# Kernel tuning notes

Hardware: AMD Instinct MI355X
Metric: run time of the kernel (lower is better)

The kernel has to match this reference:

```python
import jax, jax.numpy as jnp
import numpy as np

B, S, D = 32, 512, 1024  # batch, seq_len, input_dim == output_dim


def setup_inputs() -> dict:
    key = jax.random.key(0)
    ks = jax.random.split(key, 13)
    std = 0.05  # tf.random_normal_initializer default stddev
    w = lambda k, shp: (jax.random.normal(k, shp, dtype=jnp.float32) * std)
    inp = {"seq_input_vec": jax.random.normal(ks[0], (B, S, D), dtype=jnp.float32)}
    names = ["Ui", "Wi", "Uf", "Wf", "Uo", "Wo", "Ug", "Wg"]
    for i, n in enumerate(names):
        inp[n] = w(ks[1 + i], (D, D))
    for n in ["bi", "bf", "bo", "bg"]:
        inp[n] = jnp.zeros((D,), dtype=jnp.float32)
    return inp


def reference(seq_input_vec, Ui, Wi, bi, Uf, Wf, bf, Uo, Wo, bo, Ug, Wg, bg):
    # seq_input_vec: [B, S, D]. Fuse the 4 input projections into one GEMM
    # over the whole sequence (mathematically identical to per-step matmuls).
    U = jnp.concatenate([Ui, Uf, Uo, Ug], axis=1)          # [D, 4D]
    W = jnp.concatenate([Wi, Wf, Wo, Wg], axis=1)          # [D, 4D]
    b = jnp.concatenate([bi, bf, bo, bg], axis=0)          # [4D]
    x_proj = jnp.einsum('bsd,de->sbe', seq_input_vec, U) + b  # [S, B, 4D]

    d = seq_input_vec.shape[-1]
    h0 = jnp.zeros((seq_input_vec.shape[0], d), dtype=seq_input_vec.dtype)
    c0 = jnp.zeros_like(h0)

    def step(carry, xp):
        c_prev, h_prev = carry
        z = xp + h_prev @ W                                 # [B, 4D]
        zi, zf, zo, zg = jnp.split(z, 4, axis=-1)
        i_t = jax.nn.sigmoid(zi)
        f_t = jax.nn.sigmoid(zf)
        o_t = jax.nn.sigmoid(zo)
        g_t = jnp.tanh(zg)
        # NOTE: original (nonstandard) math applies sigmoid to the cell update
        c_t = jax.nn.sigmoid(f_t * c_prev + i_t * g_t)
        h_t = jnp.tanh(c_t) * o_t
        return (c_t, h_t), h_t

    _, hs = jax.lax.scan(step, (c0, h0), x_proj)            # hs: [S, B, D]
    return jnp.transpose(hs, (1, 0, 2))                     # [B, S, D]
```

## Files before the change

### kernel.cpp

```cpp
#include <hip/hip_runtime.h>

typedef unsigned int u32;
typedef unsigned short u16;
typedef unsigned long long u64;
typedef __attribute__((ext_vector_type(8))) short short8;
typedef __attribute__((ext_vector_type(4))) float f32x4;

#define SEQ 512
#define BATCH 32
#define DIM 1024
#define NB 128

#define OFF_XT    0ull
#define OFF_UBT   33554432ull
#define OFF_WG2   41943040ull
#define OFF_XPROJ 50331648ull
#define OFF_HBUF  184549376ull
#define OFF_BIAS  184680448ull
#define OFF_SYNC  184696832ull

__device__ __forceinline__ float bf2f(u16 u) {
  union { u32 u; float f; } v; v.u = ((u32)u) << 16; return v.f;
}
__device__ __forceinline__ u16 f2bf(float f) {
  union { float f; u32 u; } v; v.f = f;
  u32 r = v.u + 0x7FFFu + ((v.u >> 16) & 1u);
  return (u16)(r >> 16);
}
__device__ __forceinline__ float tanh_fast(float x) {
  return 1.f - 2.f / (1.f + __expf(2.f * x));
}
__device__ __forceinline__ void gload_lds16(const u16* g, u16* l) {
  __builtin_amdgcn_global_load_lds(
      (const __attribute__((address_space(1))) u32*)g,
      (__attribute__((address_space(3))) u32*)l, 16, 0, 0);
}
__device__ __forceinline__ void gload_lds16_coh(const u16* g, u16* l) {
  __builtin_amdgcn_global_load_lds(
      (const __attribute__((address_space(1))) u32*)g,
      (__attribute__((address_space(3))) u32*)l, 16, 0, 17);
}

__global__ void k_init(u32* hb, float* biasc, u32* sync,
                       const float* bi, const float* bfv,
                       const float* bo, const float* bg) {
  int i = blockIdx.x * 256 + threadIdx.x;
  if (i < 32768) {
    hb[i] = 0u;
  } else if (i < 32768 + 4096) {
    int e = i - 32768;
    int g = e >> 10, c = e & 1023;
    const float* p = (g == 0) ? bi : (g == 1) ? bfv : (g == 2) ? bo : bg;
    biasc[e] = p[c];
  } else if (i < 32768 + 4096 + 4096) {
    sync[i - 32768 - 4096] = 0u;
  }
}

__global__ void k_prep_w(const float* Ui, const float* Wi, const float* Uf,
                         const float* Wf, const float* Uo, const float* Wo,
                         const float* Ug, const float* Wg, u16* Ubt, u16* Wg2) {
  __shared__ float tile[64][65];
  int bx = blockIdx.x;
  int mi = bx >> 8;
  int tt = bx & 255;
  int tr = tt >> 4, tc = tt & 15;
  const float* src;
  switch (mi) {
    case 0: src = Ui; break; case 1: src = Wi; break;
    case 2: src = Uf; break; case 3: src = Wf; break;
    case 4: src = Uo; break; case 5: src = Wo; break;
    case 6: src = Ug; break; default: src = Wg; break;
  }
  int g = mi >> 1;
  int d0 = tr * 64, c0 = tc * 64;
  int ty = threadIdx.x >> 6, tx = threadIdx.x & 63;
#pragma unroll
  for (int i = 0; i < 16; ++i) {
    int r = i * 4 + ty;
    tile[r][tx] = src[(size_t)(d0 + r) * 1024 + c0 + tx];
  }
  __syncthreads();
  if (mi & 1) {
#pragma unroll
    for (int i = 0; i < 16; ++i) {
      int cc = i * 4 + ty;
      int c_full = c0 + cc;
      int k = d0 + tx;
      int blk = c_full >> 3;
      int rr = (g << 3) | (c_full & 7);
      Wg2[(size_t)blk * 32768 + ((k >> 5) << 10) + rr * 32 + (k & 31)] =
          f2bf(tile[tx][cc]);
    }
  } else {
#pragma unroll
    for (int i = 0; i < 16; ++i) {
      int cc = i * 4 + ty;
      Ubt[(size_t)((g << 10) + c0 + cc) * 1024 + d0 + tx] = f2bf(tile[tx][cc]);
    }
  }
}

__global__ void k_prep_x(const float* __restrict__ X, u16* __restrict__ Xt) {
  int idx = blockIdx.x * 256 + threadIdx.x;
  int m = idx >> 8, d4 = (idx & 255) << 2;
  int s = m >> 5, b = m & 31;
  const float4* p = (const float4*)(X + (size_t)(b * SEQ + s) * DIM + d4);
  float4 v = *p;
  u16 o[4] = { f2bf(v.x), f2bf(v.y), f2bf(v.z), f2bf(v.w) };
  *(ushort4*)(Xt + (size_t)m * DIM + d4) = *(ushort4*)o;
}

__global__ __launch_bounds__(256) void k_gemm(const u16* __restrict__ Xt,
                                              const u16* __restrict__ Ubt,
                                              const float* __restrict__ biasc,
                                              u16* __restrict__ xproj) {
  __shared__ u16 As[128 * 32];
  __shared__ u16 Bs[128 * 32];
  int tid = threadIdx.x;
  int w = tid >> 6, l = tid & 63;
  int n0 = blockIdx.x * 128, m0 = blockIdx.y * 128;
  int wm = w >> 1, wn = w & 1;
  int lrow = l & 15, lq = l >> 4;
  f32x4 acc[4][4] = {};
  for (int kt = 0; kt < 32; ++kt) {
    int k0 = kt * 32;
    __syncthreads();
#pragma unroll
    for (int is = 0; is < 2; ++is) {
      int c = is * 256 + w * 64 + l;
      int row = c >> 2, kg = c & 3;
      gload_lds16(Xt + (size_t)(m0 + row) * 1024 + k0 + kg * 8, As + c * 8);
      gload_lds16(Ubt + (size_t)(n0 + row) * 1024 + k0 + kg * 8, Bs + c * 8);
    }
    __syncthreads();
    short8 af[4], bf[4];
#pragma unroll
    for (int mt = 0; mt < 4; ++mt)
      af[mt] = *(const short8*)(As + (wm * 64 + mt * 16 + lrow) * 32 + lq * 8);
#pragma unroll
    for (int nt = 0; nt < 4; ++nt)
      bf[nt] = *(const short8*)(Bs + (wn * 64 + nt * 16 + lrow) * 32 + lq * 8);
#pragma unroll
    for (int mt = 0; mt < 4; ++mt)
#pragma unroll
      for (int nt = 0; nt < 4; ++nt)
        acc[mt][nt] = __builtin_amdgcn_mfma_f32_16x16x32_bf16(
            af[mt], bf[nt], acc[mt][nt], 0, 0, 0);
  }
#pragma unroll
  for (int nt = 0; nt < 4; ++nt) {
    int col = n0 + wn * 64 + nt * 16 + lrow;
    float bv = biasc[col];
#pragma unroll
    for (int mt = 0; mt < 4; ++mt) {
      int rbase = m0 + wm * 64 + mt * 16 + lq * 4;
#pragma unroll
      for (int r = 0; r < 4; ++r)
        xproj[(size_t)(rbase + r) * 4096 + col] = f2bf(acc[mt][nt][r] + bv);
    }
  }
}

__global__ __launch_bounds__(256, 1) void k_rec(const u16* __restrict__ Wg2,
                                                const u16* __restrict__ xproj,
                                                u16* hbuf, float* out, u32* sync) {
  __shared__ u16 Ws[32 * 1024];
  __shared__ u16 Hs[32 * 1024];
  __shared__ u16 XPs[32 * 32];
  __shared__ float zbuf[32][33];
  int tid = threadIdx.x;
  int w = tid >> 6, l = tid & 63;
  int blk = blockIdx.x;
  int lrow = l & 15, lq = l >> 4;
#pragma unroll
  for (int it = 0; it < 16; ++it) {
    int c = it * 256 + w * 64 + l;
    gload_lds16(Wg2 + (size_t)blk * 32768 + c * 8, Ws + c * 8);
  }
  if (w < 2) {
    int c2 = w * 64 + l;
    int b = c2 >> 2, g = c2 & 3;
    gload_lds16(xproj + (size_t)b * 4096 + (g << 10) + (blk << 3), XPs + c2 * 8);
  }
  float c_reg = 0.f;
  int eb = tid >> 3, ec = tid & 7;
  int mt = w >> 1, nt = w & 1;
  const u16* ap0 = Hs + (mt * 16 + lrow) * 32 + lq * 8;
  const u16* bp0 = Ws + (nt * 16 + lrow) * 32 + lq * 8;
  u16* hst_base = hbuf + ((blk >> 2) << 10) + eb * 32 + ((blk & 3) << 3) + ec;
  float* out_base = out + (size_t)eb * SEQ * DIM + (blk << 3) + ec;
  __syncthreads();

  for (int s = 0; s < SEQ; ++s) {
    {
      u32 tgt = (u32)s;
      int guard = 0;
      for (;;) {
        u32 a = __hip_atomic_load(sync + l * 32, __ATOMIC_RELAXED,
                                  __HIP_MEMORY_SCOPE_AGENT);
        u32 b = __hip_atomic_load(sync + (64 + l) * 32, __ATOMIC_RELAXED,
                                  __HIP_MEMORY_SCOPE_AGENT);
        if (a >= tgt && b >= tgt) break;
        __builtin_amdgcn_s_sleep(1);
        if (++guard > 20000000) break;
      }
    }
    asm volatile("" ::: "memory");

    const u16* hsrc = hbuf + (size_t)(s & 1) * 32768;
#pragma unroll
    for (int it = 0; it < 16; ++it) {
      int c = it * 256 + w * 64 + l;
      gload_lds16_coh(hsrc + c * 8, Hs + c * 8);
    }
    asm volatile("s_waitcnt vmcnt(8)" ::: "memory");
    __builtin_amdgcn_s_barrier();
    __builtin_amdgcn_sched_barrier(0);

    f32x4 acc0 = { 0.f, 0.f, 0.f, 0.f };
    f32x4 acc1 = { 0.f, 0.f, 0.f, 0.f };
#pragma unroll
    for (int ks = 0; ks < 8; ++ks) {
      short8 a0 = *(const short8*)(ap0 + (2 * ks) * 1024);
      short8 b0 = *(const short8*)(bp0 + (2 * ks) * 1024);
      short8 a1 = *(const short8*)(ap0 + (2 * ks + 1) * 1024);
      short8 b1 = *(const short8*)(bp0 + (2 * ks + 1) * 1024);
      acc0 = __builtin_amdgcn_mfma_f32_16x16x32_bf16(a0, b0, acc0, 0, 0, 0);
      acc1 = __builtin_amdgcn_mfma_f32_16x16x32_bf16(a1, b1, acc1, 0, 0, 0);
    }
    asm volatile("s_waitcnt vmcnt(0)" ::: "memory");
    __builtin_amdgcn_s_barrier();
    __builtin_amdgcn_sched_barrier(0);
#pragma unroll
    for (int ks = 8; ks < 16; ++ks) {
      short8 a0 = *(const short8*)(ap0 + (2 * ks) * 1024);
      short8 b0 = *(const short8*)(bp0 + (2 * ks) * 1024);
      short8 a1 = *(const short8*)(ap0 + (2 * ks + 1) * 1024);
      short8 b1 = *(const short8*)(bp0 + (2 * ks + 1) * 1024);
      acc0 = __builtin_amdgcn_mfma_f32_16x16x32_bf16(a0, b0, acc0, 0, 0, 0);
      acc1 = __builtin_amdgcn_mfma_f32_16x16x32_bf16(a1, b1, acc1, 0, 0, 0);
    }
    f32x4 acc = acc0 + acc1;
    {
      int col = nt * 16 + lrow;
      int rb = mt * 16 + lq * 4;
#pragma unroll
      for (int r = 0; r < 4; ++r) zbuf[rb + r][col] = acc[r];
    }
    __syncthreads();

    float zi = zbuf[eb][ec]      + bf2f(XPs[eb * 32 + ec]);
    float zf = zbuf[eb][8 + ec]  + bf2f(XPs[eb * 32 + 8 + ec]);
    float zo = zbuf[eb][16 + ec] + bf2f(XPs[eb * 32 + 16 + ec]);
    float zg = zbuf[eb][24 + ec] + bf2f(XPs[eb * 32 + 24 + ec]);
    float ig = 1.f / (1.f + __expf(-zi));
    float fg = 1.f / (1.f + __expf(-zf));
    float og = 1.f / (1.f + __expf(-zo));
    float gg = tanh_fast(zg);
    c_reg = 1.f / (1.f + __expf(-(fg * c_reg + ig * gg)));
    float h = tanh_fast(c_reg) * og;
    __hip_atomic_store(hst_base + (size_t)(((s + 1) & 1)) * 32768, f2bf(h),
                       __ATOMIC_RELAXED, __HIP_MEMORY_SCOPE_AGENT);
    __syncthreads();

    if (tid == 0)
      __hip_atomic_store(sync + blk * 32, (u32)(s + 1), __ATOMIC_RELAXED,
                         __HIP_MEMORY_SCOPE_AGENT);
    {
      int sp = (s + 1 < SEQ) ? s + 1 : s;
      if (w < 2) {
        int c2 = w * 64 + l;
        int b = c2 >> 2, g = c2 & 3;
        gload_lds16(xproj + (size_t)(sp * 32 + b) * 4096 + (g << 10) + (blk << 3),
                    XPs + c2 * 8);
      }
    }
    __builtin_nontemporal_store(h, out_base + (size_t)s * DIM);
  }
}

extern "C" void kernel_launch(void* const* d_in, const int* in_sizes, int n_in,
                              void* d_out, int out_size, void* d_ws,
                              size_t ws_size, hipStream_t stream) {
  const float* X   = (const float*)d_in[0];
  const float* Ui  = (const float*)d_in[1];
  const float* Wi  = (const float*)d_in[2];
  const float* Uf  = (const float*)d_in[3];
  const float* Wf  = (const float*)d_in[4];
  const float* Uo  = (const float*)d_in[5];
  const float* Wo  = (const float*)d_in[6];
  const float* Ug  = (const float*)d_in[7];
  const float* Wg  = (const float*)d_in[8];
  const float* bi  = (const float*)d_in[9];
  const float* bfv = (const float*)d_in[10];
  const float* bo  = (const float*)d_in[11];
  const float* bg  = (const float*)d_in[12];
  char* ws = (char*)d_ws;
  u16* Xt      = (u16*)(ws + OFF_XT);
  u16* Ubt     = (u16*)(ws + OFF_UBT);
  u16* Wg2     = (u16*)(ws + OFF_WG2);
  u16* xproj   = (u16*)(ws + OFF_XPROJ);
  u16* hbuf    = (u16*)(ws + OFF_HBUF);
  float* biasc = (float*)(ws + OFF_BIAS);
  u32* sync    = (u32*)(ws + OFF_SYNC);
  float* out   = (float*)d_out;

  k_init<<<160, 256, 0, stream>>>((u32*)hbuf, biasc, sync, bi, bfv, bo, bg);
  k_prep_w<<<2048, 256, 0, stream>>>(Ui, Wi, Uf, Wf, Uo, Wo, Ug, Wg, Ubt, Wg2);
  k_prep_x<<<16384, 256, 0, stream>>>(X, Xt);
  k_gemm<<<dim3(32, 128), 256, 0, stream>>>(Xt, Ubt, biasc, xproj);
  k_rec<<<NB, 256, 0, stream>>>(Wg2, xproj, hbuf, out, sync);
}
```

Before: 1.948 ms.

## Split recurrent block into two independent batch halves with per-half sync

The recurrent kernel now splits each block's 256 threads into two 128-thread groups, each handling 16 of the 32 batch rows. Each group waits on its own set of global step flags, loads only its half of h, and synchronises its two waves through an LDS flag spin instead of block-wide barriers. This lets the two batch halves advance through the sequence independently, so the cross-block dependency chain covers only half the batch. The cost is more flag traffic, spin-waiting on LDS flags, and double-buffered xproj staging. The bf array is also renamed to avoid shadowing a variable name.

Measured after the change: 2.688 ms. 38.0% more time.

```diff
diff --git a/kernel.cpp b/kernel.cpp
--- a/kernel.cpp
+++ b/kernel.cpp
@@ -39,6 +39,19 @@
   __builtin_amdgcn_global_load_lds(
       (const __attribute__((address_space(1))) u32*)g,
       (__attribute__((address_space(3))) u32*)l, 16, 0, 17);
+}
+
+__device__ __forceinline__ void half_sync(volatile u32* hsf, int g, int wv,
+                                          u32 ep) {
+  asm volatile("s_waitcnt lgkmcnt(0)" ::: "memory");
+  if ((threadIdx.x & 63) == 0) hsf[g * 2 + wv] = ep;
+  asm volatile("s_waitcnt lgkmcnt(0)" ::: "memory");
+  int guard = 0;
+  while (hsf[g * 2 + (wv ^ 1)] < ep) {
+    if (++guard > 100000000) break;
+  }
+  asm volatile("" ::: "memory");
+  __builtin_amdgcn_sched_barrier(0);
 }
 
 __global__ void k_init(u32* hb, float* biasc, u32* sync,
@@ -134,19 +147,19 @@
       gload_lds16(Ubt + (size_t)(n0 + row) * 1024 + k0 + kg * 8, Bs + c * 8);
     }
     __syncthreads();
-    short8 af[4], bf[4];
+    short8 af[4], bfr[4];
 #pragma unroll
     for (int mt = 0; mt < 4; ++mt)
       af[mt] = *(const short8*)(As + (wm * 64 + mt * 16 + lrow) * 32 + lq * 8);
 #pragma unroll
     for (int nt = 0; nt < 4; ++nt)
-      bf[nt] = *(const short8*)(Bs + (wn * 64 + nt * 16 + lrow) * 32 + lq * 8);
+      bfr[nt] = *(const short8*)(Bs + (wn * 64 + nt * 16 + lrow) * 32 + lq * 8);
 #pragma unroll
     for (int mt = 0; mt < 4; ++mt)
 #pragma unroll
       for (int nt = 0; nt < 4; ++nt)
         acc[mt][nt] = __builtin_amdgcn_mfma_f32_16x16x32_bf16(
-            af[mt], bf[nt], acc[mt][nt], 0, 0, 0);
+            af[mt], bfr[nt], acc[mt][nt], 0, 0, 0);
   }
 #pragma unroll
   for (int nt = 0; nt < 4; ++nt) {
@@ -166,30 +179,36 @@
                                                 const u16* __restrict__ xproj,
                                                 u16* hbuf, float* out, u32* sync) {
   __shared__ u16 Ws[32 * 1024];
-  __shared__ u16 Hs[32 * 1024];
-  __shared__ u16 XPs[32 * 32];
-  __shared__ float zbuf[32][33];
+  __shared__ u16 Hs[2][16 * 1024];
+  __shared__ u16 XPs[2][2][512];
+  __shared__ float zb[2][16][33];
+  __shared__ u32 hsf[4];
   int tid = threadIdx.x;
   int w = tid >> 6, l = tid & 63;
+  int g = tid >> 7;
+  int wv = w & 1;
   int blk = blockIdx.x;
   int lrow = l & 15, lq = l >> 4;
+  if (tid < 4) hsf[tid] = 0u;
 #pragma unroll
   for (int it = 0; it < 16; ++it) {
     int c = it * 256 + w * 64 + l;
     gload_lds16(Wg2 + (size_t)blk * 32768 + c * 8, Ws + c * 8);
   }
-  if (w < 2) {
-    int c2 = w * 64 + l;
-    int b = c2 >> 2, g = c2 & 3;
-    gload_lds16(xproj + (size_t)b * 4096 + (g << 10) + (blk << 3), XPs + c2 * 8);
+  {
+    int bloc = l >> 2, gs = l & 3;
+    gload_lds16(xproj + (size_t)(g * 16 + bloc) * 4096 + gs * 1024 + (blk << 3),
+                &XPs[g][0][l * 8]);
   }
   float c_reg = 0.f;
-  int eb = tid >> 3, ec = tid & 7;
-  int mt = w >> 1, nt = w & 1;
-  const u16* ap0 = Hs + (mt * 16 + lrow) * 32 + lq * 8;
-  const u16* bp0 = Ws + (nt * 16 + lrow) * 32 + lq * 8;
-  u16* hst_base = hbuf + ((blk >> 2) << 10) + eb * 32 + ((blk & 3) << 3) + ec;
-  float* out_base = out + (size_t)eb * SEQ * DIM + (blk << 3) + ec;
+  int eb = (tid & 127) >> 3, ec = tid & 7;
+  const u16* ap0 = Hs[g] + lrow * 32 + lq * 8;
+  const u16* bp0 = Ws + (wv * 16 + lrow) * 32 + lq * 8;
+  int d = (blk << 3) + ec;
+  u16* hst_base = hbuf + ((d >> 5) << 10) + (g * 16 + eb) * 32 + (d & 31);
+  float* out_base = out + (size_t)(g * 16 + eb) * SEQ * DIM + d;
+  const u32* syncg = sync + g * 2048;
+  u32 epc = 0;
   __syncthreads();
 
   for (int s = 0; s < SEQ; ++s) {
@@ -197,9 +216,9 @@
       u32 tgt = (u32)s;
       int guard = 0;
       for (;;) {
-        u32 a = __hip_atomic_load(sync + l * 32, __ATOMIC_RELAXED,
+        u32 a = __hip_atomic_load(syncg + l * 16, __ATOMIC_RELAXED,
                                   __HIP_MEMORY_SCOPE_AGENT);
-        u32 b = __hip_atomic_load(sync + (64 + l) * 32, __ATOMIC_RELAXED,
+        u32 b = __hip_atomic_load(syncg + (64 + l) * 16, __ATOMIC_RELAXED,
                                   __HIP_MEMORY_SCOPE_AGENT);
         if (a >= tgt && b >= tgt) break;
         __builtin_amdgcn_s_sleep(1);
@@ -208,75 +227,66 @@
     }
     asm volatile("" ::: "memory");
 
-    const u16* hsrc = hbuf + (size_t)(s & 1) * 32768;
-#pragma unroll
-    for (int it = 0; it < 16; ++it) {
-      int c = it * 256 + w * 64 + l;
-      gload_lds16_coh(hsrc + c * 8, Hs + c * 8);
-    }
-    asm volatile("s_waitcnt vmcnt(8)" ::: "memory");
-    __builtin_amdgcn_s_barrier();
+    const u16* hsrc = hbuf + (size_t)(s & 1) * 32768 + g * 512 + l * 8;
+#pragma unroll
+    for (int t = 0; t < 16; ++t) {
+      int tile = wv * 16 + t;
+      gload_lds16_coh(hsrc + tile * 1024, Hs[g] + tile * 512 + l * 8);
+    }
+    asm volatile("s_waitcnt vmcnt(0)" ::: "memory");
     __builtin_amdgcn_sched_barrier(0);
+    half_sync(hsf, g, wv, ++epc);
 
     f32x4 acc0 = { 0.f, 0.f, 0.f, 0.f };
     f32x4 acc1 = { 0.f, 0.f, 0.f, 0.f };
 #pragma unroll
-    for (int ks = 0; ks < 8; ++ks) {
-      short8 a0 = *(const short8*)(ap0 + (2 * ks) * 1024);
-      short8 b0 = *(const short8*)(bp0 + (2 * ks) * 1024);
-      short8 a1 = *(const short8*)(ap0 + (2 * ks + 1) * 1024);
-      short8 b1 = *(const short8*)(bp0 + (2 * ks + 1) * 1024);
+    for (int kk = 0; kk < 16; ++kk) {
+      short8 a0 = *(const short8*)(ap0 + (2 * kk) * 512);
+      short8 b0 = *(const short8*)(bp0 + (2 * kk) * 1024);
+      short8 a1 = *(const short8*)(ap0 + (2 * kk + 1) * 512);
+      short8 b1 = *(const short8*)(bp0 + (2 * kk + 1) * 1024);
       acc0 = __builtin_amdgcn_mfma_f32_16x16x32_bf16(a0, b0, acc0, 0, 0, 0);
       acc1 = __builtin_amdgcn_mfma_f32_16x16x32_bf16(a1, b1, acc1, 0, 0, 0);
     }
-    asm volatile("s_waitcnt vmcnt(0)" ::: "memory");
-    __builtin_amdgcn_s_barrier();
-    __builtin_amdgcn_sched_barrier(0);
-#pragma unroll
-    for (int ks = 8; ks < 16; ++ks) {
-      short8 a0 = *(const short8*)(ap0 + (2 * ks) * 1024);
-      short8 b0 = *(const short8*)(bp0 + (2 * ks) * 1024);
-      short8 a1 = *(const short8*)(ap0 + (2 * ks + 1) * 1024);
-      short8 b1 = *(const short8*)(bp0 + (2 * ks + 1) * 1024);
-      acc0 = __builtin_amdgcn_mfma_f32_16x16x32_bf16(a0, b0, acc0, 0, 0, 0);
-      acc1 = __builtin_amdgcn_mfma_f32_16x16x32_bf16(a1, b1, acc1, 0, 0, 0);
-    }
     f32x4 acc = acc0 + acc1;
     {
-      int col = nt * 16 + lrow;
-      int rb = mt * 16 + lq * 4;
-#pragma unroll
-      for (int r = 0; r < 4; ++r) zbuf[rb + r][col] = acc[r];
-    }
-    __syncthreads();
-
-    float zi = zbuf[eb][ec]      + bf2f(XPs[eb * 32 + ec]);
-    float zf = zbuf[eb][8 + ec]  + bf2f(XPs[eb * 32 + 8 + ec]);
-    float zo = zbuf[eb][16 + ec] + bf2f(XPs[eb * 32 + 16 + ec]);
-    float zg = zbuf[eb][24 + ec] + bf2f(XPs[eb * 32 + 24 + ec]);
+      int col = wv * 16 + lrow;
+      int rb = lq * 4;
+#pragma unroll
+      for (int r = 0; r < 4; ++r) zb[g][rb + r][col] = acc[r];
+    }
+    half_sync(hsf, g, wv, ++epc);
+
+    const u16* xp = XPs[g][s & 1];
+    float zi = zb[g][eb][ec]      + bf2f(xp[eb * 32 + ec]);
+    float zf = zb[g][eb][8 + ec]  + bf2f(xp[eb * 32 + 8 + ec]);
+    float zo = zb[g][eb][16 + ec] + bf2f(xp[eb * 32 + 16 + ec]);
+    float zg = zb[g][eb][24 + ec] + bf2f(xp[eb * 32 + 24 + ec]);
     float ig = 1.f / (1.f + __expf(-zi));
     float fg = 1.f / (1.f + __expf(-zf));
     float og = 1.f / (1.f + __expf(-zo));
     float gg = tanh_fast(zg);
     c_reg = 1.f / (1.f + __expf(-(fg * c_reg + ig * gg)));
     float h = tanh_fast(c_reg) * og;
-    __hip_atomic_store(hst_base + (size_t)(((s + 1) & 1)) * 32768, f2bf(h),
+
+    __hip_atomic_store(hst_base + (size_t)((s + 1) & 1) * 32768, f2bf(h),
                        __ATOMIC_RELAXED, __HIP_MEMORY_SCOPE_AGENT);
-    __syncthreads();
-
-    if (tid == 0)
-      __hip_atomic_store(sync + blk * 32, (u32)(s + 1), __ATOMIC_RELAXED,
-                         __HIP_MEMORY_SCOPE_AGENT);
+    asm volatile("" ::: "memory");
+    __builtin_nontemporal_store(h, out_base + (size_t)s * DIM);
+    asm volatile("" ::: "memory");
     {
       int sp = (s + 1 < SEQ) ? s + 1 : s;
-      if (w < 2) {
-        int c2 = w * 64 + l;
-        int b = c2 >> 2, g = c2 & 3;
-        gload_lds16(xproj + (size_t)(sp * 32 + b) * 4096 + (g << 10) + (blk << 3),
-                    XPs + c2 * 8);
-      }
-    }
-    __builtin_nontemporal_store(h, out_base + (size_t)s * DIM);
+      int bloc = l >> 2, gs = l & 3;
+      gload_lds16(xproj + (size_t)(sp * 32 + g * 16 + bloc) * 4096 +
+                      gs * 1024 + (blk << 3),
+                  &XPs[g][(s + 1) & 1][l * 8]);
+    }
+    asm volatile("s_waitcnt vmcnt(2)" ::: "memory");
+    __builtin_amdgcn_sched_barrier(0);
+    half_sync(hsf, g, wv, ++epc);
+    if (tid == g * 128)
+      __hip_atomic_store(sync + (g * 128 + blk) * 16, (u32)(s + 1),
+                         __ATOMIC_RELAXED, __HIP_MEMORY_SCOPE_AGENT);
   }
 }
 
```

## Restructure recurrent kernel to single wave with MFMA-native layouts and deferred output

Applied to the files above, without the earlier changes.

The recurrent kernel now runs one 64-lane wave per block, with weights and x-projection pre-permuted so each lane owns four gate-tuples directly from MFMA accumulators. This removes the LDS zbuf round trip and the intra-block barriers. Hidden states for all steps go to a full history buffer that reuses the Xt workspace, with zero h0 kept in the reused Ubt region. A separate kernel converts that history to the fp32 output afterwards, taking the output stores off the serial critical path. The x-projection for the next step is prefetched into registers, and the spin-wait guard limit is lowered, which risks a premature exit if another block stalls.

After: 3.251 ms. 1.67x slower.

```diff
diff --git a/kernel.cpp b/kernel.cpp
--- a/kernel.cpp
+++ b/kernel.cpp
@@ -5,6 +5,7 @@
 typedef unsigned long long u64;
 typedef __attribute__((ext_vector_type(8))) short short8;
 typedef __attribute__((ext_vector_type(4))) float f32x4;
+typedef __attribute__((ext_vector_type(4))) u32 u32x4;
 
 #define SEQ 512
 #define BATCH 32
@@ -15,7 +16,6 @@
 #define OFF_UBT   33554432ull
 #define OFF_WG2   41943040ull
 #define OFF_XPROJ 50331648ull
-#define OFF_HBUF  184549376ull
 #define OFF_BIAS  184680448ull
 #define OFF_SYNC  184696832ull
 
@@ -41,20 +41,20 @@
       (__attribute__((address_space(3))) u32*)l, 16, 0, 17);
 }
 
-__global__ void k_init(u32* hb, float* biasc, u32* sync,
-                       const float* bi, const float* bfv,
-                       const float* bo, const float* bg) {
+__global__ void k_init(float* biasc, u32* sync, const float* bi,
+                       const float* bfv, const float* bo, const float* bg) {
   int i = blockIdx.x * 256 + threadIdx.x;
-  if (i < 32768) {
-    hb[i] = 0u;
-  } else if (i < 32768 + 4096) {
-    int e = i - 32768;
-    int g = e >> 10, c = e & 1023;
+  if (i < 4096) {
+    int g = i >> 10, c = i & 1023;
     const float* p = (g == 0) ? bi : (g == 1) ? bfv : (g == 2) ? bo : bg;
-    biasc[e] = p[c];
-  } else if (i < 32768 + 4096 + 4096) {
-    sync[i - 32768 - 4096] = 0u;
-  }
+    biasc[i] = p[c];
+  } else if (i < 8192) {
+    sync[i - 4096] = 0u;
+  }
+}
+
+__global__ void k_zero(u32x4* p) {
+  p[blockIdx.x * 256 + threadIdx.x] = (u32x4){0u, 0u, 0u, 0u};
 }
 
 __global__ void k_prep_w(const float* Ui, const float* Wi, const float* Uf,
@@ -88,9 +88,11 @@
       int c_full = c0 + cc;
       int k = d0 + tx;
       int blk = c_full >> 3;
-      int rr = (g << 3) | (c_full & 7);
-      Wg2[(size_t)blk * 32768 + ((k >> 5) << 10) + rr * 32 + (k & 31)] =
-          f2bf(tile[tx][cc]);
+      int lane = (((k & 31) >> 3) << 4) + ((c_full & 3) << 2) + g;
+      size_t idx = (size_t)blk * 32768 +
+                   (size_t)(((k >> 5) * 2 + ((c_full & 7) >> 2)) * 64 + lane) * 8 +
+                   (k & 7);
+      Wg2[idx] = f2bf(tile[tx][cc]);
     }
   } else {
 #pragma unroll
@@ -114,7 +116,7 @@
 __global__ __launch_bounds__(256) void k_gemm(const u16* __restrict__ Xt,
                                               const u16* __restrict__ Ubt,
                                               const float* __restrict__ biasc,
-                                              u16* __restrict__ xproj) {
+                                              u16* __restrict__ xp2) {
   __shared__ u16 As[128 * 32];
   __shared__ u16 Bs[128 * 32];
   int tid = threadIdx.x;
@@ -134,63 +136,67 @@
       gload_lds16(Ubt + (size_t)(n0 + row) * 1024 + k0 + kg * 8, Bs + c * 8);
     }
     __syncthreads();
-    short8 af[4], bf[4];
+    short8 af[4], bfr[4];
 #pragma unroll
     for (int mt = 0; mt < 4; ++mt)
       af[mt] = *(const short8*)(As + (wm * 64 + mt * 16 + lrow) * 32 + lq * 8);
 #pragma unroll
     for (int nt = 0; nt < 4; ++nt)
-      bf[nt] = *(const short8*)(Bs + (wn * 64 + nt * 16 + lrow) * 32 + lq * 8);
+      bfr[nt] = *(const short8*)(Bs + (wn * 64 + nt * 16 + lrow) * 32 + lq * 8);
 #pragma unroll
     for (int mt = 0; mt < 4; ++mt)
 #pragma unroll
       for (int nt = 0; nt < 4; ++nt)
         acc[mt][nt] = __builtin_amdgcn_mfma_f32_16x16x32_bf16(
-            af[mt], bf[nt], acc[mt][nt], 0, 0, 0);
+            af[mt], bfr[nt], acc[mt][nt], 0, 0, 0);
   }
 #pragma unroll
   for (int nt = 0; nt < 4; ++nt) {
     int col = n0 + wn * 64 + nt * 16 + lrow;
     float bv = biasc[col];
+    int g = col >> 10, d = col & 1023;
+    int blkd = d >> 3;
+    int slot = ((d & 7) >> 2) * 4 + g;
+    int lpart = (d & 3) * 16;
 #pragma unroll
     for (int mt = 0; mt < 4; ++mt) {
       int rbase = m0 + wm * 64 + mt * 16 + lq * 4;
 #pragma unroll
-      for (int r = 0; r < 4; ++r)
-        xproj[(size_t)(rbase + r) * 4096 + col] = f2bf(acc[mt][nt][r] + bv);
-    }
-  }
-}
-
-__global__ __launch_bounds__(256, 1) void k_rec(const u16* __restrict__ Wg2,
-                                                const u16* __restrict__ xproj,
-                                                u16* hbuf, float* out, u32* sync) {
-  __shared__ u16 Ws[32 * 1024];
-  __shared__ u16 Hs[32 * 1024];
-  __shared__ u16 XPs[32 * 32];
-  __shared__ float zbuf[32][33];
-  int tid = threadIdx.x;
-  int w = tid >> 6, l = tid & 63;
+      for (int r = 0; r < 4; ++r) {
+        int row = rbase + r;
+        int s = row >> 5, b = row & 31;
+        xp2[(size_t)(s * 128 + blkd) * 1024 + (lpart + (b & 15)) * 16 +
+            (b >> 4) * 8 + slot] = f2bf(acc[mt][nt][r] + bv);
+      }
+    }
+  }
+}
+
+__global__ __launch_bounds__(64, 1) void k_rec(const u16* __restrict__ Wg2,
+                                               const u16* __restrict__ xp2,
+                                               u16* hX, const u16* __restrict__ h0,
+                                               u32* sync) {
+  __shared__ u16 Ws[32768];
+  __shared__ u16 Hs[32768];
+  int l = threadIdx.x;
   int blk = blockIdx.x;
-  int lrow = l & 15, lq = l >> 4;
-#pragma unroll
-  for (int it = 0; it < 16; ++it) {
-    int c = it * 256 + w * 64 + l;
-    gload_lds16(Wg2 + (size_t)blk * 32768 + c * 8, Ws + c * 8);
-  }
-  if (w < 2) {
-    int c2 = w * 64 + l;
-    int b = c2 >> 2, g = c2 & 3;
-    gload_lds16(xproj + (size_t)b * 4096 + (g << 10) + (blk << 3), XPs + c2 * 8);
-  }
-  float c_reg = 0.f;
-  int eb = tid >> 3, ec = tid & 7;
-  int mt = w >> 1, nt = w & 1;
-  const u16* ap0 = Hs + (mt * 16 + lrow) * 32 + lq * 8;
-  const u16* bp0 = Ws + (nt * 16 + lrow) * 32 + lq * 8;
-  u16* hst_base = hbuf + ((blk >> 2) << 10) + eb * 32 + ((blk & 3) << 3) + ec;
-  float* out_base = out + (size_t)eb * SEQ * DIM + (blk << 3) + ec;
-  __syncthreads();
+#pragma unroll
+  for (int it = 0; it < 64; ++it)
+    gload_lds16(Wg2 + (size_t)blk * 32768 + it * 512 + l * 8,
+                Ws + it * 512 + l * 8);
+  u32x4 xqc0, xqc1, xqn0, xqn1;
+  {
+    const u16* xp = xp2 + (size_t)blk * 1024 + l * 16;
+    asm volatile("global_load_dwordx4 %0, %1, off" : "=v"(xqc0) : "v"(xp));
+    asm volatile("global_load_dwordx4 %0, %1, off" : "=v"(xqc1) : "v"(xp + 8));
+  }
+  asm volatile("s_waitcnt vmcnt(0)" ::: "memory");
+  __builtin_amdgcn_sched_barrier(0);
+
+  int q = l >> 4, b15 = l & 15;
+  int hoff0 = (((blk >> 2) * 2 + 0) * 64 + (blk & 3) * 16 + b15) * 8 + q;
+  int hoff1 = (((blk >> 2) * 2 + 1) * 64 + (blk & 3) * 16 + b15) * 8 + q;
+  float c00 = 0.f, c01 = 0.f, c10 = 0.f, c11 = 0.f;
 
   for (int s = 0; s < SEQ; ++s) {
     {
@@ -203,81 +209,106 @@
                                   __HIP_MEMORY_SCOPE_AGENT);
         if (a >= tgt && b >= tgt) break;
         __builtin_amdgcn_s_sleep(1);
-        if (++guard > 20000000) break;
+        if (++guard > 1000000) break;
       }
     }
     asm volatile("" ::: "memory");
-
-    const u16* hsrc = hbuf + (size_t)(s & 1) * 32768;
-#pragma unroll
-    for (int it = 0; it < 16; ++it) {
-      int c = it * 256 + w * 64 + l;
-      gload_lds16_coh(hsrc + c * 8, Hs + c * 8);
-    }
-    asm volatile("s_waitcnt vmcnt(8)" ::: "memory");
-    __builtin_amdgcn_s_barrier();
-    __builtin_amdgcn_sched_barrier(0);
-
-    f32x4 acc0 = { 0.f, 0.f, 0.f, 0.f };
-    f32x4 acc1 = { 0.f, 0.f, 0.f, 0.f };
-#pragma unroll
-    for (int ks = 0; ks < 8; ++ks) {
-      short8 a0 = *(const short8*)(ap0 + (2 * ks) * 1024);
-      short8 b0 = *(const short8*)(bp0 + (2 * ks) * 1024);
-      short8 a1 = *(const short8*)(ap0 + (2 * ks + 1) * 1024);
-      short8 b1 = *(const short8*)(bp0 + (2 * ks + 1) * 1024);
-      acc0 = __builtin_amdgcn_mfma_f32_16x16x32_bf16(a0, b0, acc0, 0, 0, 0);
-      acc1 = __builtin_amdgcn_mfma_f32_16x16x32_bf16(a1, b1, acc1, 0, 0, 0);
-    }
+    __builtin_amdgcn_sched_barrier(0);
+
+    const u16* hs = (s == 0) ? h0 : (hX + (size_t)(s - 1) * 32768);
+#pragma unroll
+    for (int g2 = 0; g2 < 64; ++g2)
+      gload_lds16_coh(hs + g2 * 512 + l * 8, Hs + g2 * 512 + l * 8);
+    {
+      int sp = (s + 1 < SEQ) ? s + 1 : s;
+      const u16* xp = xp2 + ((size_t)sp * 128 + blk) * 1024 + l * 16;
+      asm volatile("global_load_dwordx4 %0, %1, off" : "=v"(xqn0) : "v"(xp));
+      asm volatile("global_load_dwordx4 %0, %1, off" : "=v"(xqn1) : "v"(xp + 8));
+    }
+
+    f32x4 a00 = {0.f,0.f,0.f,0.f}, a01 = {0.f,0.f,0.f,0.f};
+    f32x4 a10 = {0.f,0.f,0.f,0.f}, a11 = {0.f,0.f,0.f,0.f};
+#define MFMA_CHUNK(KT0, KT1)                                               \
+    _Pragma("unroll")                                                      \
+    for (int kt = (KT0); kt < (KT1); ++kt) {                               \
+      short8 w0 = *(const short8*)(Ws + (kt * 2 + 0) * 512 + l * 8);       \
+      short8 w1 = *(const short8*)(Ws + (kt * 2 + 1) * 512 + l * 8);       \
+      short8 b0 = *(const short8*)(Hs + (kt * 2 + 0) * 512 + l * 8);       \
+      short8 b1 = *(const short8*)(Hs + (kt * 2 + 1) * 512 + l * 8);       \
+      a00 = __builtin_amdgcn_mfma_f32_16x16x32_bf16(w0, b0, a00, 0, 0, 0); \
+      a01 = __builtin_amdgcn_mfma_f32_16x16x32_bf16(w0, b1, a01, 0, 0, 0); \
+      a10 = __builtin_amdgcn_mfma_f32_16x16x32_bf16(w1, b0, a10, 0, 0, 0); \
+      a11 = __builtin_amdgcn_mfma_f32_16x16x32_bf16(w1, b1, a11, 0, 0, 0); \
+    }
+    asm volatile("s_waitcnt vmcnt(50)" ::: "memory");
+    __builtin_amdgcn_sched_barrier(0);
+    MFMA_CHUNK(0, 8)
+    asm volatile("s_waitcnt vmcnt(34)" ::: "memory");
+    __builtin_amdgcn_sched_barrier(0);
+    MFMA_CHUNK(8, 16)
+    asm volatile("s_waitcnt vmcnt(18)" ::: "memory");
+    __builtin_amdgcn_sched_barrier(0);
+    MFMA_CHUNK(16, 24)
+    asm volatile("s_waitcnt vmcnt(2)" ::: "memory");
+    __builtin_amdgcn_sched_barrier(0);
+    MFMA_CHUNK(24, 32)
+#undef MFMA_CHUNK
+
+    union { u32x4 v[2]; u16 a[16]; } xq;
+    xq.v[0] = xqc0; xq.v[1] = xqc1;
+    float h00, h01, h10, h11;
+#define CELL(AC, CR, HV, CT, RT)                                           \
+    {                                                                      \
+      float zi = AC[0] + bf2f(xq.a[(CT)*8 + (RT)*4 + 0]);                  \
+      float zf = AC[1] + bf2f(xq.a[(CT)*8 + (RT)*4 + 1]);                  \
+      float zo = AC[2] + bf2f(xq.a[(CT)*8 + (RT)*4 + 2]);                  \
+      float zg = AC[3] + bf2f(xq.a[(CT)*8 + (RT)*4 + 3]);                  \
+      float ig = 1.f / (1.f + __expf(-zi));                                \
+      float fg = 1.f / (1.f + __expf(-zf));                                \
+      float og = 1.f / (1.f + __expf(-zo));                                \
+      float gg = tanh_fast(zg);                                            \
+      CR = 1.f / (1.f + __expf(-(fg * CR + ig * gg)));                     \
+      HV = tanh_fast(CR) * og;                                             \
+    }
+    CELL(a00, c00, h00, 0, 0)
+    CELL(a01, c01, h01, 1, 0)
+    CELL(a10, c10, h10, 0, 1)
+    CELL(a11, c11, h11, 1, 1)
+#undef CELL
+
+    u16* hn = hX + (size_t)s * 32768;
+    __hip_atomic_store(hn + hoff0,     f2bf(h00), __ATOMIC_RELAXED,
+                       __HIP_MEMORY_SCOPE_AGENT);
+    __hip_atomic_store(hn + hoff1,     f2bf(h01), __ATOMIC_RELAXED,
+                       __HIP_MEMORY_SCOPE_AGENT);
+    __hip_atomic_store(hn + hoff0 + 4, f2bf(h10), __ATOMIC_RELAXED,
+                       __HIP_MEMORY_SCOPE_AGENT);
+    __hip_atomic_store(hn + hoff1 + 4, f2bf(h11), __ATOMIC_RELAXED,
+                       __HIP_MEMORY_SCOPE_AGENT);
     asm volatile("s_waitcnt vmcnt(0)" ::: "memory");
-    __builtin_amdgcn_s_barrier();
-    __builtin_amdgcn_sched_barrier(0);
-#pragma unroll
-    for (int ks = 8; ks < 16; ++ks) {
-      short8 a0 = *(const short8*)(ap0 + (2 * ks) * 1024);
-      short8 b0 = *(const short8*)(bp0 + (2 * ks) * 1024);
-      short8 a1 = *(const short8*)(ap0 + (2 * ks + 1) * 1024);
-      short8 b1 = *(const short8*)(bp0 + (2 * ks + 1) * 1024);
-      acc0 = __builtin_amdgcn_mfma_f32_16x16x32_bf16(a0, b0, acc0, 0, 0, 0);
-      acc1 = __builtin_amdgcn_mfma_f32_16x16x32_bf16(a1, b1, acc1, 0, 0, 0);
-    }
-    f32x4 acc = acc0 + acc1;
-    {
-      int col = nt * 16 + lrow;
-      int rb = mt * 16 + lq * 4;
-#pragma unroll
-      for (int r = 0; r < 4; ++r) zbuf[rb + r][col] = acc[r];
-    }
-    __syncthreads();
-
-    float zi = zbuf[eb][ec]      + bf2f(XPs[eb * 32 + ec]);
-    float zf = zbuf[eb][8 + ec]  + bf2f(XPs[eb * 32 + 8 + ec]);
-    float zo = zbuf[eb][16 + ec] + bf2f(XPs[eb * 32 + 16 + ec]);
-    float zg = zbuf[eb][24 + ec] + bf2f(XPs[eb * 32 + 24 + ec]);
-    float ig = 1.f / (1.f + __expf(-zi));
-    float fg = 1.f / (1.f + __expf(-zf));
-    float og = 1.f / (1.f + __expf(-zo));
-    float gg = tanh_fast(zg);
-    c_reg = 1.f / (1.f + __expf(-(fg * c_reg + ig * gg)));
-    float h = tanh_fast(c_reg) * og;
-    __hip_atomic_store(hst_base + (size_t)(((s + 1) & 1)) * 32768, f2bf(h),
-                       __ATOMIC_RELAXED, __HIP_MEMORY_SCOPE_AGENT);
-    __syncthreads();
-
-    if (tid == 0)
+    __builtin_amdgcn_sched_barrier(0);
+    if (l == 0)
       __hip_atomic_store(sync + blk * 32, (u32)(s + 1), __ATOMIC_RELAXED,
                          __HIP_MEMORY_SCOPE_AGENT);
-    {
-      int sp = (s + 1 < SEQ) ? s + 1 : s;
-      if (w < 2) {
-        int c2 = w * 64 + l;
-        int b = c2 >> 2, g = c2 & 3;
-        gload_lds16(xproj + (size_t)(sp * 32 + b) * 4096 + (g << 10) + (blk << 3),
-                    XPs + c2 * 8);
-      }
-    }
-    __builtin_nontemporal_store(h, out_base + (size_t)s * DIM);
-  }
+    xqc0 = xqn0; xqc1 = xqn1;
+  }
+}
+
+__global__ void k_out(const u16* __restrict__ hx, float* __restrict__ out) {
+  int t = blockIdx.x * 256 + threadIdx.x;
+  int d0 = (t & 127) << 3;
+  int rem = t >> 7;
+  int s = rem & 511, b = rem >> 9;
+  int kt = d0 >> 5, jg = (d0 & 31) >> 3, ct = b >> 4;
+  const u16* src = hx + (size_t)s * 32768 +
+                   (size_t)(((kt * 2 + ct) * 64 + jg * 16 + (b & 15)) * 8);
+  ushort4 v0 = *(const ushort4*)src;
+  ushort4 v1 = *(const ushort4*)(src + 4);
+  float4 o0 = { bf2f(v0.x), bf2f(v0.y), bf2f(v0.z), bf2f(v0.w) };
+  float4 o1 = { bf2f(v1.x), bf2f(v1.y), bf2f(v1.z), bf2f(v1.w) };
+  float* dst = out + (size_t)(b * SEQ + s) * DIM + d0;
+  *(float4*)dst = o0;
+  *(float4*)(dst + 4) = o1;
 }
 
 extern "C" void kernel_launch(void* const* d_in, const int* in_sizes, int n_in,
@@ -300,15 +331,16 @@
   u16* Xt      = (u16*)(ws + OFF_XT);
   u16* Ubt     = (u16*)(ws + OFF_UBT);
   u16* Wg2     = (u16*)(ws + OFF_WG2);
-  u16* xproj   = (u16*)(ws + OFF_XPROJ);
-  u16* hbuf    = (u16*)(ws + OFF_HBUF);
+  u16* xp2     = (u16*)(ws + OFF_XPROJ);
   float* biasc = (float*)(ws + OFF_BIAS);
   u32* sync    = (u32*)(ws + OFF_SYNC);
   float* out   = (float*)d_out;
 
-  k_init<<<160, 256, 0, stream>>>((u32*)hbuf, biasc, sync, bi, bfv, bo, bg);
+  k_init<<<32, 256, 0, stream>>>(biasc, sync, bi, bfv, bo, bg);
   k_prep_w<<<2048, 256, 0, stream>>>(Ui, Wi, Uf, Wf, Uo, Wo, Ug, Wg, Ubt, Wg2);
   k_prep_x<<<16384, 256, 0, stream>>>(X, Xt);
-  k_gemm<<<dim3(32, 128), 256, 0, stream>>>(Xt, Ubt, biasc, xproj);
-  k_rec<<<NB, 256, 0, stream>>>(Wg2, xproj, hbuf, out, sync);
-}
+  k_gemm<<<dim3(32, 128), 256, 0, stream>>>(Xt, Ubt, biasc, xp2);
+  k_zero<<<16, 256, 0, stream>>>((u32x4*)Ubt);
+  k_rec<<<NB, 64, 0, stream>>>(Wg2, xp2, Xt, Ubt, sync);
+  k_out<<<8192, 256, 0, stream>>>(Xt, out);
+}
```
